# Kernel tuning notes

Hardware: AMD Instinct MI355X
Metric: run time of the kernel (lower is better)

The kernel has to match this reference:

```python
import jax, jax.numpy as jnp
import numpy as np

D = 1024
H = 8
DK = D // H
BS, NSEG, NSEN = 16, 64, 32


def _linear_params(key, d_in, d_out, scale=0.02):
    kw, kb = jax.random.split(key)
    w = jax.random.normal(kw, (d_out, d_in), dtype=jnp.float32) * scale
    b = jax.random.normal(kb, (d_out,), dtype=jnp.float32) * scale
    return w, b


def setup_inputs() -> dict:
    key = jax.random.key(0)
    ks = jax.random.split(key, 12)
    A = jax.random.normal(ks[0], (BS, NSEG, D), dtype=jnp.float32)
    V = jax.random.normal(ks[1], (BS, NSEG, D), dtype=jnp.float32)
    S = jax.random.normal(ks[2], (BS, NSEN, D), dtype=jnp.float32)
    wA, bA = _linear_params(ks[3], D, D)
    wV, bV = _linear_params(ks[4], D, D)
    wS, bS = _linear_params(ks[5], D, D)
    wq, bq = _linear_params(ks[6], D, D)
    wk, bk = _linear_params(ks[7], D, D)
    wv, bv = _linear_params(ks[8], D, D)
    w1, b1 = _linear_params(ks[9], D, D)
    w2, b2 = _linear_params(ks[10], D, D)
    return {"A": A, "V": V, "S": S,
            "wA": wA, "bA": bA, "wV": wV, "bV": bV, "wS": wS, "bS": bS,
            "wq": wq, "bq": bq, "wk": wk, "bk": bk, "wv": wv, "bv": bv,
            "w1": w1, "b1": b1, "w2": w2, "b2": b2}


def _lin(x, w, b):
    return x @ w.T + b


def reference(A, V, S, wA, bA, wV, bV, wS, bS, wq, bq, wk, bk, wv, bv, w1, b1, w2, b2):
    bs, num_seg, d_model = A.shape
    num_sen = S.shape[1]
    A = _lin(A, wA, bA)
    V = _lin(V, wV, bV)
    S = _lin(S, wS, bS)
    av = jnp.stack([A, V], axis=2)                       # (bs, num_seg, 2, d)
    q = _lin(S, wq, bq).reshape(bs, num_sen, H, DK)      # (b, s, h, dk)
    k = _lin(av, wk, bk).reshape(bs, num_seg, 2, H, DK)  # (b, g, a, h, dk)
    v = _lin(av, wv, bv).reshape(bs, num_seg, 2, H, DK)
    # attention over the size-2 A/V axis only
    attn = jnp.einsum('bshd,bgahd->bsgah', q, k) / np.sqrt(DK).astype(np.float32)
    attn = jax.nn.softmax(attn, axis=3)                  # softmax over a (A vs V)
    out = jnp.einsum('bsgah,bgahd->bsghd', attn, v)
    out = out.reshape(bs, num_sen, num_seg, d_model)
    # positionwise FF: Linear -> ReLU -> Linear (dropout p=0)
    out = _lin(jax.nn.relu(_lin(out, w1, b1)), w2, b2)
    return out
```

## Files before the change

### kernel.cpp

```cpp
#include <hip/hip_runtime.h>
#include <stdint.h>


#define D_MODEL 1024
#define N_HEAD  8
#define DK      128
#define BS      16
#define NSEG    64
#define NSEN    32

typedef __attribute__((ext_vector_type(8))) __bf16 bf16x8;
typedef __attribute__((ext_vector_type(8))) unsigned short u16x8;
typedef __attribute__((ext_vector_type(4))) float f32x4;

__device__ __forceinline__ float bf2f(unsigned short b) {
  union { unsigned int u; float f; } x; x.u = ((unsigned int)b) << 16; return x.f;
}
__device__ __forceinline__ unsigned short f2bf(float f) {
  union { float f; unsigned int u; } x; x.f = f;
  unsigned int u = x.u;
  unsigned int r = (u + 0x7fffu + ((u >> 16) & 1u)) >> 16;
  return (unsigned short)r;
}

__device__ __forceinline__ void g2l16(const void* g, void* l) {
  __builtin_amdgcn_global_load_lds(
      (const __attribute__((address_space(1))) void*)g,
      (__attribute__((address_space(3))) void*)l, 16, 0, 0);
}

struct CvtB { const float* s[11]; unsigned short* d[11]; int n4[11]; };
__global__ __launch_bounds__(256)
void cvtall_kernel(CvtB p) {
  const int z = blockIdx.y;
  const int i = blockIdx.x * 256 + threadIdx.x;
  if (i >= p.n4[z]) return;
  float4 v = reinterpret_cast<const float4*>(p.s[z])[i];
  ushort4 o;
  o.x = f2bf(v.x); o.y = f2bf(v.y); o.z = f2bf(v.z); o.w = f2bf(v.w);
  reinterpret_cast<ushort4*>(p.d[z])[i] = o;
}

struct GSeg { const unsigned short* A; const unsigned short* B;
              const float* bias; unsigned short* C; };
struct GBatch { GSeg s[3]; int end[3]; };

__global__ __launch_bounds__(256)
void gemm64_bt(GBatch gb) {
  __shared__ __align__(16) unsigned short lA[64 * 32];
  __shared__ __align__(16) unsigned short lB[128 * 32];

  const int nwg = gridDim.x;
  const int sw = (blockIdx.x & 7) * (nwg >> 3) + (blockIdx.x >> 3);
  int sgi = 0, base = 0;
  if (sw >= gb.end[0]) { sgi = 1; base = gb.end[0]; }
  if (sw >= gb.end[1]) { sgi = 2; base = gb.end[1]; }
  const GSeg sg = gb.s[sgi];
  const int st = sw - base;
  const int m0 = (st >> 3) * 64, n0 = (st & 7) * 128;

  const int t = threadIdx.x;
  const int lane = t & 63, w = t >> 6;
  const int fr = lane & 15, kg = lane >> 4;

  f32x4 acc[4][2] = {};

  const int r  = t >> 2;
  const int c8 = (t & 3) * 8;
  const unsigned short* ga  = sg.A + (size_t)(m0 + r) * 1024 + c8;
  const unsigned short* gbp = sg.B + (size_t)(n0 + r) * 1024 + c8;

  for (int k0 = 0; k0 < 1024; k0 += 32) {
    __syncthreads();
    g2l16(ga + k0,              &lA[t * 8]);
    g2l16(gbp + k0,             &lB[t * 8]);
    g2l16(gbp + k0 + 64 * 1024, &lB[2048 + t * 8]);
    __syncthreads();

    u16x8 af[4], bf[2];
#pragma unroll
    for (int mi = 0; mi < 4; ++mi)
      af[mi] = *reinterpret_cast<const u16x8*>(&lA[(mi * 16 + fr) * 32 + kg * 8]);
#pragma unroll
    for (int ni = 0; ni < 2; ++ni)
      bf[ni] = *reinterpret_cast<const u16x8*>(&lB[(w * 32 + ni * 16 + fr) * 32 + kg * 8]);
#pragma unroll
    for (int mi = 0; mi < 4; ++mi)
#pragma unroll
      for (int ni = 0; ni < 2; ++ni)
        acc[mi][ni] = __builtin_amdgcn_mfma_f32_16x16x32_bf16(
            __builtin_bit_cast(bf16x8, af[mi]), __builtin_bit_cast(bf16x8, bf[ni]),
            acc[mi][ni], 0, 0, 0);
  }

#pragma unroll
  for (int ni = 0; ni < 2; ++ni) {
    const int gn = n0 + w * 32 + ni * 16 + fr;
    const float bv = sg.bias[gn];
#pragma unroll
    for (int mi = 0; mi < 4; ++mi) {
      const int gm = m0 + mi * 16 + kg * 4;
#pragma unroll
      for (int j = 0; j < 4; ++j)
        sg.C[(size_t)(gm + j) * 1024 + gn] = f2bf(acc[mi][ni][j] + bv);
    }
  }
}

__global__ __launch_bounds__(512, 2)
void gemm8p_bt(const unsigned short* __restrict__ A, const unsigned short* __restrict__ B,
               const float* __restrict__ bias, float* __restrict__ C,
               int M, int N, int K, int nbx) {
  __shared__ __align__(16) unsigned short lds[2][2][256][64];

  const int nwg = gridDim.x;
  const int sw = (blockIdx.x & 7) * (nwg >> 3) + (blockIdx.x >> 3);
  const int m0 = (sw / nbx) * 256, n0 = (sw % nbx) * 256;

  const int T = threadIdx.x;
  const int lane = T & 63, wave = T >> 6;
  const int wr = wave >> 2, wc = wave & 3;
  const int fr = lane & 15, kg = lane >> 4;
  const int NT = K >> 6;

  const int sgs = (T & 7) ^ ((T >> 3) & 7);
  int grA[2][2], grB[2][2];
#pragma unroll
  for (int mh = 0; mh < 2; ++mh)
#pragma unroll
    for (int c = 0; c < 2; ++c) {
      int l = mh * 128 + c * 64 + (T >> 3);
      grA[mh][c] = ((l >> 6) & 1) * 128 + (l >> 7) * 64 + (l & 63);
      grB[mh][c] = ((l >> 5) & 3) * 64  + (l >> 7) * 32 + (l & 31);
    }
  const unsigned short* Abase = A + (size_t)m0 * K + sgs * 8;
  const unsigned short* Bbase = B + (size_t)n0 * K + sgs * 8;
  char* ldsc = (char*)&lds[0][0][0][0];

  auto stageA = [&](int buf, int mh, int t) {
#pragma unroll
    for (int c = 0; c < 2; ++c)
      g2l16(Abase + (size_t)grA[mh][c] * K + t * 64,
            ldsc + ((size_t)buf * 65536) + (mh * 128 + c * 64) * 128 + T * 16);
  };
  auto stageB = [&](int buf, int nh, int t) {
#pragma unroll
    for (int c = 0; c < 2; ++c)
      g2l16(Bbase + (size_t)grB[nh][c] * K + t * 64,
            ldsc + ((size_t)buf * 65536) + 32768 + (nh * 128 + c * 64) * 128 + T * 16);
  };

  int koff[2];
#pragma unroll
  for (int kk = 0; kk < 2; ++kk) koff[kk] = ((kk * 4 + kg) ^ (fr & 7)) * 16;
  int lrA[8], lrB[4];
#pragma unroll
  for (int mi = 0; mi < 8; ++mi) lrA[mi] = ((mi >> 2) * 128 + wr * 64 + (mi & 3) * 16 + fr) * 128;
#pragma unroll
  for (int ni = 0; ni < 4; ++ni) lrB[ni] = ((ni >> 1) * 128 + wc * 32 + (ni & 1) * 16 + fr) * 128;

  auto rdA = [&](int buf, int mi, int kk) -> u16x8 {
    return *reinterpret_cast<const u16x8*>(ldsc + (size_t)buf * 65536 + lrA[mi] + koff[kk]);
  };
  auto rdB = [&](int buf, int ni, int kk) -> u16x8 {
    return *reinterpret_cast<const u16x8*>(ldsc + (size_t)buf * 65536 + 32768 + lrB[ni] + koff[kk]);
  };

  f32x4 acc[8][4] = {};

  stageA(0, 0, 0); stageB(0, 0, 0); stageA(0, 1, 0); stageB(0, 1, 0);
  if (NT > 1) { stageA(1, 0, 1); stageB(1, 0, 1); stageA(1, 1, 1); }
  asm volatile("s_waitcnt vmcnt(6)" ::: "memory");
  __builtin_amdgcn_s_barrier();

  u16x8 af0[4][2], af1[4][2], bf0[2][2], bf1[2][2];

  for (int t = 0; t < NT; ++t) {
    const int buf = t & 1;
    const bool st1 = (t + 1 < NT), st2 = (t + 2 < NT);

#pragma unroll
    for (int mi = 0; mi < 4; ++mi)
#pragma unroll
      for (int kk = 0; kk < 2; ++kk) af0[mi][kk] = rdA(buf, mi, kk);
#pragma unroll
    for (int ni = 0; ni < 2; ++ni)
#pragma unroll
      for (int kk = 0; kk < 2; ++kk) bf0[ni][kk] = rdB(buf, ni, kk);
    if (st1) stageB(buf ^ 1, 1, t + 1);
    __builtin_amdgcn_s_barrier();
    asm volatile("s_waitcnt lgkmcnt(0)" ::: "memory");
    __builtin_amdgcn_sched_barrier(0);
    __builtin_amdgcn_s_setprio(1);
#pragma unroll
    for (int mi = 0; mi < 4; ++mi)
#pragma unroll
      for (int ni = 0; ni < 2; ++ni)
#pragma unroll
        for (int kk = 0; kk < 2; ++kk)
          acc[mi][ni] = __builtin_amdgcn_mfma_f32_16x16x32_bf16(
              __builtin_bit_cast(bf16x8, af0[mi][kk]), __builtin_bit_cast(bf16x8, bf0[ni][kk]),
              acc[mi][ni], 0, 0, 0);
    __builtin_amdgcn_s_setprio(0);
    __builtin_amdgcn_s_barrier();

#pragma unroll
    for (int mi = 0; mi < 4; ++mi)
#pragma unroll
      for (int kk = 0; kk < 2; ++kk) af1[mi][kk] = rdA(buf, mi + 4, kk);
#pragma unroll
    for (int ni = 0; ni < 2; ++ni)
#pragma unroll
      for (int kk = 0; kk < 2; ++kk) bf1[ni][kk] = rdB(buf, ni + 2, kk);
    if (st2) stageA(buf, 0, t + 2);
    __builtin_amdgcn_s_barrier();
    asm volatile("s_waitcnt lgkmcnt(0)" ::: "memory");
    __builtin_amdgcn_sched_barrier(0);
    __builtin_amdgcn_s_setprio(1);
#pragma unroll
    for (int mi = 0; mi < 4; ++mi)
#pragma unroll
      for (int ni = 0; ni < 2; ++ni)
#pragma unroll
        for (int kk = 0; kk < 2; ++kk)
          acc[mi][ni + 2] = __builtin_amdgcn_mfma_f32_16x16x32_bf16(
              __builtin_bit_cast(bf16x8, af0[mi][kk]), __builtin_bit_cast(bf16x8, bf1[ni][kk]),
              acc[mi][ni + 2], 0, 0, 0);
    __builtin_amdgcn_s_setprio(0);
    __builtin_amdgcn_s_barrier();

    if (st2) stageB(buf, 0, t + 2);
    __builtin_amdgcn_s_barrier();
    __builtin_amdgcn_s_setprio(1);
#pragma unroll
    for (int mi = 0; mi < 4; ++mi)
#pragma unroll
      for (int ni = 0; ni < 2; ++ni)
#pragma unroll
        for (int kk = 0; kk < 2; ++kk)
          acc[mi + 4][ni + 2] = __builtin_amdgcn_mfma_f32_16x16x32_bf16(
              __builtin_bit_cast(bf16x8, af1[mi][kk]), __builtin_bit_cast(bf16x8, bf1[ni][kk]),
              acc[mi + 4][ni + 2], 0, 0, 0);
    __builtin_amdgcn_s_setprio(0);
    __builtin_amdgcn_s_barrier();

    if (st2) stageA(buf, 1, t + 2);
    __builtin_amdgcn_s_barrier();
    __builtin_amdgcn_s_setprio(1);
#pragma unroll
    for (int mi = 0; mi < 4; ++mi)
#pragma unroll
      for (int ni = 0; ni < 2; ++ni)
#pragma unroll
        for (int kk = 0; kk < 2; ++kk)
          acc[mi + 4][ni] = __builtin_amdgcn_mfma_f32_16x16x32_bf16(
              __builtin_bit_cast(bf16x8, af1[mi][kk]), __builtin_bit_cast(bf16x8, bf0[ni][kk]),
              acc[mi + 4][ni], 0, 0, 0);
    __builtin_amdgcn_s_setprio(0);
    if (st2)       asm volatile("s_waitcnt vmcnt(6)" ::: "memory");
    else if (st1)  asm volatile("s_waitcnt vmcnt(0)" ::: "memory");
    __builtin_amdgcn_s_barrier();
  }

#pragma unroll
  for (int ni = 0; ni < 4; ++ni) {
    const int gn = n0 + wc * 64 + ni * 16 + fr;
    const float bv = bias[gn];
#pragma unroll
    for (int mi = 0; mi < 8; ++mi) {
      const int gm = m0 + wr * 128 + mi * 16 + kg * 4;
#pragma unroll
      for (int j = 0; j < 4; ++j)
        C[(size_t)(gm + j) * N + gn] = acc[mi][ni][j] + bv;
    }
  }
}

__global__ __launch_bounds__(256)
void uav_gemm(const unsigned short* __restrict__ vAV, const unsigned short* __restrict__ w1,
              unsigned short* __restrict__ UAV) {
  __shared__ __align__(16) unsigned short lA[128 * 32];
  __shared__ __align__(16) unsigned short lB[128 * 32];

  const int zb = blockIdx.z;
  const int tensor = zb >> 3, h = zb & 7;
  const unsigned short* Ab = vAV + (size_t)tensor * (1024 * 1024) + h * 128;
  const unsigned short* Bb = w1 + h * 128;
  unsigned short* Cb = UAV + (size_t)tensor * (1024 * 8192) + h * 1024;

  const int t = threadIdx.x;
  const int m0 = blockIdx.y * 128, n0 = blockIdx.x * 128;
  const int lane = t & 63, wv = t >> 6;
  const int wrow = (wv >> 1) * 64, wcol = (wv & 1) * 64;
  const int fr = lane & 15, kg = lane >> 4;

  f32x4 acc[4][4] = {};

  const int r  = t >> 2;
  const int c8 = (t & 3) * 8;
  const unsigned short* ga = Ab + (size_t)(m0 + r) * 1024 + c8;
  const unsigned short* gb = Bb + (size_t)(n0 + r) * 1024 + c8;

  for (int k0 = 0; k0 < 128; k0 += 32) {
    __syncthreads();
    g2l16(ga + k0,             &lA[t * 8]);
    g2l16(ga + k0 + 64 * 1024, &lA[2048 + t * 8]);
    g2l16(gb + k0,             &lB[t * 8]);
    g2l16(gb + k0 + 64 * 1024, &lB[2048 + t * 8]);
    __syncthreads();

    u16x8 af[4], bg_[4];
#pragma unroll
    for (int mi = 0; mi < 4; ++mi)
      af[mi] = *reinterpret_cast<const u16x8*>(&lA[(wrow + mi * 16 + fr) * 32 + kg * 8]);
#pragma unroll
    for (int ni = 0; ni < 4; ++ni)
      bg_[ni] = *reinterpret_cast<const u16x8*>(&lB[(wcol + ni * 16 + fr) * 32 + kg * 8]);
#pragma unroll
    for (int mi = 0; mi < 4; ++mi)
#pragma unroll
      for (int ni = 0; ni < 4; ++ni)
        acc[mi][ni] = __builtin_amdgcn_mfma_f32_16x16x32_bf16(
            __builtin_bit_cast(bf16x8, af[mi]), __builtin_bit_cast(bf16x8, bg_[ni]),
            acc[mi][ni], 0, 0, 0);
  }

  const int rg = kg * 4;
#pragma unroll
  for (int ni = 0; ni < 4; ++ni) {
    const int gn = n0 + wcol + ni * 16 + fr;
#pragma unroll
    for (int mi = 0; mi < 4; ++mi) {
      const int gm = m0 + wrow + mi * 16 + rg;
#pragma unroll
      for (int j = 0; j < 4; ++j)
        Cb[(size_t)(gm + j) * 8192 + gn] = f2bf(acc[mi][ni][j]);
    }
  }
}

__global__ __launch_bounds__(256)
void score_hid_kernel(const unsigned short* __restrict__ q,
                      const unsigned short* __restrict__ kAV,
                      const unsigned short* __restrict__ UAV,
                      const float* __restrict__ b1,
                      unsigned short* __restrict__ hid) {
  const int bg = blockIdx.x;
  const int b = bg >> 6, g = bg & 63;
  __shared__ float sk[2][D_MODEL];
  __shared__ float pAl[NSEN][N_HEAD];
  const size_t rowA = (size_t)bg * D_MODEL;
  const size_t rowV = rowA + (size_t)BS * NSEG * D_MODEL;
  for (int i = threadIdx.x; i < D_MODEL; i += 256) {
    sk[0][i] = bf2f(kAV[rowA + i]);
    sk[1][i] = bf2f(kAV[rowV + i]);
  }
  __syncthreads();

  const int h = threadIdx.x >> 5;
  const int l = threadIdx.x & 31;
  const float scale = 0.08838834764831845f;

  for (int s = 0; s < NSEN; ++s) {
    const unsigned short* pq = q + ((size_t)(b * NSEN + s)) * D_MODEL + h * DK;
    float la = 0.f, lv = 0.f;
#pragma unroll
    for (int e = 0; e < 4; ++e) {
      int d = l + e * 32;
      float qv = bf2f(pq[d]);
      la += qv * sk[0][h * DK + d];
      lv += qv * sk[1][h * DK + d];
    }
#pragma unroll
    for (int off = 16; off; off >>= 1) {
      la += __shfl_xor(la, off, 32);
      lv += __shfl_xor(lv, off, 32);
    }
    if (l == 0) pAl[s][h] = 1.f / (1.f + __expf((lv - la) * scale));
  }
  __syncthreads();

  const int n0 = threadIdx.x * 4;
  const unsigned short* ua = UAV + (size_t)bg * 8192 + n0;
  const unsigned short* uv = ua + (size_t)1024 * 8192;

  float dU[N_HEAD][4];
  float base[4];
#pragma unroll
  for (int j = 0; j < 4; ++j) base[j] = b1[n0 + j];
#pragma unroll
  for (int hh = 0; hh < N_HEAD; ++hh) {
    ushort4 a4 = *reinterpret_cast<const ushort4*>(ua + hh * 1024);
    ushort4 v4 = *reinterpret_cast<const ushort4*>(uv + hh * 1024);
    float va[4] = {bf2f(a4.x), bf2f(a4.y), bf2f(a4.z), bf2f(a4.w)};
    float vv[4] = {bf2f(v4.x), bf2f(v4.y), bf2f(v4.z), bf2f(v4.w)};
#pragma unroll
    for (int j = 0; j < 4; ++j) { dU[hh][j] = va[j] - vv[j]; base[j] += vv[j]; }
  }

  for (int s = 0; s < NSEN; ++s) {
    float val[4] = {base[0], base[1], base[2], base[3]};
#pragma unroll
    for (int hh = 0; hh < N_HEAD; ++hh) {
      const float p = pAl[s][hh];
#pragma unroll
      for (int j = 0; j < 4; ++j) val[j] = fmaf(p, dU[hh][j], val[j]);
    }
    ushort4 o;
    o.x = f2bf(val[0] > 0.f ? val[0] : 0.f);
    o.y = f2bf(val[1] > 0.f ? val[1] : 0.f);
    o.z = f2bf(val[2] > 0.f ? val[2] : 0.f);
    o.w = f2bf(val[3] > 0.f ? val[3] : 0.f);
    size_t orow = ((size_t)(b * NSEN + s) * NSEG + g) * D_MODEL + n0;
    *reinterpret_cast<ushort4*>(hid + orow) = o;
  }
}

extern "C" void kernel_launch(void* const* d_in, const int* in_sizes, int n_in,
                              void* d_out, int out_size, void* d_ws, size_t ws_size,
                              hipStream_t stream) {
  const float* A  = (const float*)d_in[0];
  const float* V  = (const float*)d_in[1];
  const float* S  = (const float*)d_in[2];
  const float* wA = (const float*)d_in[3];  const float* bA = (const float*)d_in[4];
  const float* wV = (const float*)d_in[5];  const float* bV = (const float*)d_in[6];
  const float* wS = (const float*)d_in[7];  const float* bS = (const float*)d_in[8];
  const float* wq = (const float*)d_in[9];  const float* bq = (const float*)d_in[10];
  const float* wk = (const float*)d_in[11]; const float* bk = (const float*)d_in[12];
  const float* wv = (const float*)d_in[13]; const float* bv = (const float*)d_in[14];
  const float* w1 = (const float*)d_in[15]; const float* b1 = (const float*)d_in[16];
  const float* w2 = (const float*)d_in[17]; const float* b2 = (const float*)d_in[18];

  const int nAV = BS * NSEG * D_MODEL;
  const int nS  = BS * NSEN * D_MODEL;
  const int nW  = D_MODEL * D_MODEL;
  const int nCT = BS * NSEN * NSEG * D_MODEL;
  const int nU  = 2 * 1024 * 8 * 1024;

  char* ws = (char*)d_ws;
  size_t off = 0;
  auto carve = [&](size_t elems) {
    unsigned short* p = (unsigned short*)(ws + off);
    off += elems * sizeof(unsigned short);
    return p;
  };
  unsigned short* bwA = carve(nW);
  unsigned short* bwV = carve(nW);
  unsigned short* bwS = carve(nW);
  unsigned short* bwq = carve(nW);
  unsigned short* bwk = carve(nW);
  unsigned short* bwv = carve(nW);
  unsigned short* bw1 = carve(nW);
  unsigned short* bw2 = carve(nW);
  unsigned short* xA  = carve(nAV);
  unsigned short* xV  = carve(nAV);
  unsigned short* xS  = carve(nS);
  unsigned short* A1V1 = carve(2 * nAV);
  unsigned short* S1  = carve(nS);
  unsigned short* qb  = carve(nS);
  unsigned short* kAV = carve(2 * nAV);
  unsigned short* vAV = carve(2 * nAV);
  unsigned short* UAV = carve(nU);
  unsigned short* hid = carve(nCT);
  (void)ws_size; (void)n_in; (void)in_sizes; (void)out_size;

  CvtB cv;
  cv.s[0] = wA; cv.d[0] = bwA; cv.n4[0] = nW / 4;
  cv.s[1] = wV; cv.d[1] = bwV; cv.n4[1] = nW / 4;
  cv.s[2] = wS; cv.d[2] = bwS; cv.n4[2] = nW / 4;
  cv.s[3] = wq; cv.d[3] = bwq; cv.n4[3] = nW / 4;
  cv.s[4] = wk; cv.d[4] = bwk; cv.n4[4] = nW / 4;
  cv.s[5] = wv; cv.d[5] = bwv; cv.n4[5] = nW / 4;
  cv.s[6] = w1; cv.d[6] = bw1; cv.n4[6] = nW / 4;
  cv.s[7] = w2; cv.d[7] = bw2; cv.n4[7] = nW / 4;
  cv.s[8] = A;  cv.d[8] = xA;  cv.n4[8] = nAV / 4;
  cv.s[9] = V;  cv.d[9] = xV;  cv.n4[9] = nAV / 4;
  cv.s[10] = S; cv.d[10] = xS; cv.n4[10] = nS / 4;
  cvtall_kernel<<<dim3(1024, 11), dim3(256), 0, stream>>>(cv);

  GBatch pj;
  pj.s[0] = {xA, bwA, bA, A1V1};        pj.end[0] = 128;
  pj.s[1] = {xV, bwV, bV, A1V1 + nAV};  pj.end[1] = 256;
  pj.s[2] = {xS, bwS, bS, S1};          pj.end[2] = 320;
  gemm64_bt<<<dim3(320), 256, 0, stream>>>(pj);

  GBatch qkv;
  qkv.s[0] = {S1,   bwq, bq, qb};   qkv.end[0] = 64;
  qkv.s[1] = {A1V1, bwk, bk, kAV};  qkv.end[1] = 320;
  qkv.s[2] = {A1V1, bwv, bv, vAV};  qkv.end[2] = 576;
  gemm64_bt<<<dim3(576), 256, 0, stream>>>(qkv);

  uav_gemm<<<dim3(8, 8, 16), dim3(256), 0, stream>>>(vAV, bw1, UAV);

  score_hid_kernel<<<dim3(BS * NSEG), dim3(256), 0, stream>>>(qb, kAV, UAV, b1, hid);

  gemm8p_bt<<<dim3(512), 512, 0, stream>>>(hid, bw2, b2, (float*)d_out,
                                           32768, 1024, 1024, 4);
}
```

Measured before the change: 198.3 us.

## Double-buffer small GEMMs and swap MFMA operands for vectorized row-contiguous stores

gemm64_bt and uav_gemm now stage the next K-slice into a second LDS buffer while computing the current one, so load latency overlaps MFMA work. All three GEMMs swap the MFMA A/B operands, which transposes the accumulator layout so each lane holds four consecutive columns. The epilogues can then use float4 bias loads and 8/16-byte vector stores instead of scalar strided stores. The large GEMM's phase order is also reshuffled so af1 is loaded later. This doubles LDS use in the small kernels, which may lower occupancy.

```diff
diff --git a/kernel.cpp b/kernel.cpp
--- a/kernel.cpp
+++ b/kernel.cpp
@@ -47,8 +47,8 @@
 
 __global__ __launch_bounds__(256)
 void gemm64_bt(GBatch gb) {
-  __shared__ __align__(16) unsigned short lA[64 * 32];
-  __shared__ __align__(16) unsigned short lB[128 * 32];
+  __shared__ __align__(16) unsigned short lA[2][64 * 32];
+  __shared__ __align__(16) unsigned short lB[2][128 * 32];
 
   const int nwg = gridDim.x;
   const int sw = (blockIdx.x & 7) * (nwg >> 3) + (blockIdx.x >> 3);
@@ -63,46 +63,59 @@
   const int lane = t & 63, w = t >> 6;
   const int fr = lane & 15, kg = lane >> 4;
 
-  f32x4 acc[4][2] = {};
+  f32x4 acc[2][4] = {};
 
   const int r  = t >> 2;
   const int c8 = (t & 3) * 8;
   const unsigned short* ga  = sg.A + (size_t)(m0 + r) * 1024 + c8;
   const unsigned short* gbp = sg.B + (size_t)(n0 + r) * 1024 + c8;
 
+  auto stage = [&](int buf, int k0) {
+    g2l16(ga + k0,              &lA[buf][t * 8]);
+    g2l16(gbp + k0,             &lB[buf][t * 8]);
+    g2l16(gbp + k0 + 64 * 1024, &lB[buf][2048 + t * 8]);
+  };
+
+  stage(0, 0);
+  asm volatile("s_waitcnt vmcnt(0)" ::: "memory");
+  __syncthreads();
+
   for (int k0 = 0; k0 < 1024; k0 += 32) {
+    const int buf = (k0 >> 5) & 1;
+    if (k0 + 32 < 1024) stage(buf ^ 1, k0 + 32);
+
+    u16x8 af[4], bf[2];
+#pragma unroll
+    for (int mi = 0; mi < 4; ++mi)
+      af[mi] = *reinterpret_cast<const u16x8*>(&lA[buf][(mi * 16 + fr) * 32 + kg * 8]);
+#pragma unroll
+    for (int ni = 0; ni < 2; ++ni)
+      bf[ni] = *reinterpret_cast<const u16x8*>(&lB[buf][(w * 32 + ni * 16 + fr) * 32 + kg * 8]);
+#pragma unroll
+    for (int ni = 0; ni < 2; ++ni)
+#pragma unroll
+      for (int mi = 0; mi < 4; ++mi)
+        acc[ni][mi] = __builtin_amdgcn_mfma_f32_16x16x32_bf16(
+            __builtin_bit_cast(bf16x8, bf[ni]), __builtin_bit_cast(bf16x8, af[mi]),
+            acc[ni][mi], 0, 0, 0);
+
+    asm volatile("s_waitcnt vmcnt(0)" ::: "memory");
     __syncthreads();
-    g2l16(ga + k0,              &lA[t * 8]);
-    g2l16(gbp + k0,             &lB[t * 8]);
-    g2l16(gbp + k0 + 64 * 1024, &lB[2048 + t * 8]);
-    __syncthreads();
-
-    u16x8 af[4], bf[2];
-#pragma unroll
-    for (int mi = 0; mi < 4; ++mi)
-      af[mi] = *reinterpret_cast<const u16x8*>(&lA[(mi * 16 + fr) * 32 + kg * 8]);
-#pragma unroll
-    for (int ni = 0; ni < 2; ++ni)
-      bf[ni] = *reinterpret_cast<const u16x8*>(&lB[(w * 32 + ni * 16 + fr) * 32 + kg * 8]);
-#pragma unroll
-    for (int mi = 0; mi < 4; ++mi)
-#pragma unroll
-      for (int ni = 0; ni < 2; ++ni)
-        acc[mi][ni] = __builtin_amdgcn_mfma_f32_16x16x32_bf16(
-            __builtin_bit_cast(bf16x8, af[mi]), __builtin_bit_cast(bf16x8, bf[ni]),
-            acc[mi][ni], 0, 0, 0);
   }
 
 #pragma unroll
   for (int ni = 0; ni < 2; ++ni) {
-    const int gn = n0 + w * 32 + ni * 16 + fr;
-    const float bv = sg.bias[gn];
+    const int gn0 = n0 + w * 32 + ni * 16 + kg * 4;
+    const float4 bv = *reinterpret_cast<const float4*>(&sg.bias[gn0]);
 #pragma unroll
     for (int mi = 0; mi < 4; ++mi) {
-      const int gm = m0 + mi * 16 + kg * 4;
-#pragma unroll
-      for (int j = 0; j < 4; ++j)
-        sg.C[(size_t)(gm + j) * 1024 + gn] = f2bf(acc[mi][ni][j] + bv);
+      const int gm = m0 + mi * 16 + fr;
+      ushort4 o;
+      o.x = f2bf(acc[ni][mi][0] + bv.x);
+      o.y = f2bf(acc[ni][mi][1] + bv.y);
+      o.z = f2bf(acc[ni][mi][2] + bv.z);
+      o.w = f2bf(acc[ni][mi][3] + bv.w);
+      *reinterpret_cast<ushort4*>(&sg.C[(size_t)gm * 1024 + gn0]) = o;
     }
   }
 }
@@ -166,7 +179,7 @@
     return *reinterpret_cast<const u16x8*>(ldsc + (size_t)buf * 65536 + 32768 + lrB[ni] + koff[kk]);
   };
 
-  f32x4 acc[8][4] = {};
+  f32x4 acc[4][8] = {};
 
   stageA(0, 0, 0); stageB(0, 0, 0); stageA(0, 1, 0); stageB(0, 1, 0);
   if (NT > 1) { stageA(1, 0, 1); stageB(1, 0, 1); stageA(1, 1, 1); }
@@ -193,21 +206,17 @@
     __builtin_amdgcn_sched_barrier(0);
     __builtin_amdgcn_s_setprio(1);
 #pragma unroll
-    for (int mi = 0; mi < 4; ++mi)
-#pragma unroll
-      for (int ni = 0; ni < 2; ++ni)
+    for (int ni = 0; ni < 2; ++ni)
+#pragma unroll
+      for (int mi = 0; mi < 4; ++mi)
 #pragma unroll
         for (int kk = 0; kk < 2; ++kk)
-          acc[mi][ni] = __builtin_amdgcn_mfma_f32_16x16x32_bf16(
-              __builtin_bit_cast(bf16x8, af0[mi][kk]), __builtin_bit_cast(bf16x8, bf0[ni][kk]),
-              acc[mi][ni], 0, 0, 0);
+          acc[ni][mi] = __builtin_amdgcn_mfma_f32_16x16x32_bf16(
+              __builtin_bit_cast(bf16x8, bf0[ni][kk]), __builtin_bit_cast(bf16x8, af0[mi][kk]),
+              acc[ni][mi], 0, 0, 0);
     __builtin_amdgcn_s_setprio(0);
     __builtin_amdgcn_s_barrier();
 
-#pragma unroll
-    for (int mi = 0; mi < 4; ++mi)
-#pragma unroll
-      for (int kk = 0; kk < 2; ++kk) af1[mi][kk] = rdA(buf, mi + 4, kk);
 #pragma unroll
     for (int ni = 0; ni < 2; ++ni)
 #pragma unroll
@@ -218,44 +227,50 @@
     __builtin_amdgcn_sched_barrier(0);
     __builtin_amdgcn_s_setprio(1);
 #pragma unroll
+    for (int ni = 0; ni < 2; ++ni)
+#pragma unroll
+      for (int mi = 0; mi < 4; ++mi)
+#pragma unroll
+        for (int kk = 0; kk < 2; ++kk)
+          acc[ni + 2][mi] = __builtin_amdgcn_mfma_f32_16x16x32_bf16(
+              __builtin_bit_cast(bf16x8, bf1[ni][kk]), __builtin_bit_cast(bf16x8, af0[mi][kk]),
+              acc[ni + 2][mi], 0, 0, 0);
+    __builtin_amdgcn_s_setprio(0);
+    __builtin_amdgcn_s_barrier();
+
+#pragma unroll
     for (int mi = 0; mi < 4; ++mi)
 #pragma unroll
-      for (int ni = 0; ni < 2; ++ni)
+      for (int kk = 0; kk < 2; ++kk) af1[mi][kk] = rdA(buf, mi + 4, kk);
+    if (st2) stageB(buf, 0, t + 2);
+    __builtin_amdgcn_s_barrier();
+    asm volatile("s_waitcnt lgkmcnt(0)" ::: "memory");
+    __builtin_amdgcn_sched_barrier(0);
+    __builtin_amdgcn_s_setprio(1);
+#pragma unroll
+    for (int ni = 0; ni < 2; ++ni)
+#pragma unroll
+      for (int mi = 0; mi < 4; ++mi)
 #pragma unroll
         for (int kk = 0; kk < 2; ++kk)
-          acc[mi][ni + 2] = __builtin_amdgcn_mfma_f32_16x16x32_bf16(
-              __builtin_bit_cast(bf16x8, af0[mi][kk]), __builtin_bit_cast(bf16x8, bf1[ni][kk]),
-              acc[mi][ni + 2], 0, 0, 0);
+          acc[ni + 2][mi + 4] = __builtin_amdgcn_mfma_f32_16x16x32_bf16(
+              __builtin_bit_cast(bf16x8, bf1[ni][kk]), __builtin_bit_cast(bf16x8, af1[mi][kk]),
+              acc[ni + 2][mi + 4], 0, 0, 0);
     __builtin_amdgcn_s_setprio(0);
     __builtin_amdgcn_s_barrier();
 
-    if (st2) stageB(buf, 0, t + 2);
+    if (st2) stageA(buf, 1, t + 2);
     __builtin_amdgcn_s_barrier();
     __builtin_amdgcn_s_setprio(1);
 #pragma unroll
-    for (int mi = 0; mi < 4; ++mi)
-#pragma unroll
-      for (int ni = 0; ni < 2; ++ni)
+    for (int ni = 0; ni < 2; ++ni)
+#pragma unroll
+      for (int mi = 0; mi < 4; ++mi)
 #pragma unroll
         for (int kk = 0; kk < 2; ++kk)
-          acc[mi + 4][ni + 2] = __builtin_amdgcn_mfma_f32_16x16x32_bf16(
-              __builtin_bit_cast(bf16x8, af1[mi][kk]), __builtin_bit_cast(bf16x8, bf1[ni][kk]),
-              acc[mi + 4][ni + 2], 0, 0, 0);
-    __builtin_amdgcn_s_setprio(0);
-    __builtin_amdgcn_s_barrier();
-
-    if (st2) stageA(buf, 1, t + 2);
-    __builtin_amdgcn_s_barrier();
-    __builtin_amdgcn_s_setprio(1);
-#pragma unroll
-    for (int mi = 0; mi < 4; ++mi)
-#pragma unroll
-      for (int ni = 0; ni < 2; ++ni)
-#pragma unroll
-        for (int kk = 0; kk < 2; ++kk)
-          acc[mi + 4][ni] = __builtin_amdgcn_mfma_f32_16x16x32_bf16(
-              __builtin_bit_cast(bf16x8, af1[mi][kk]), __builtin_bit_cast(bf16x8, bf0[ni][kk]),
-              acc[mi + 4][ni], 0, 0, 0);
+          acc[ni][mi + 4] = __builtin_amdgcn_mfma_f32_16x16x32_bf16(
+              __builtin_bit_cast(bf16x8, bf0[ni][kk]), __builtin_bit_cast(bf16x8, af1[mi][kk]),
+              acc[ni][mi + 4], 0, 0, 0);
     __builtin_amdgcn_s_setprio(0);
     if (st2)       asm volatile("s_waitcnt vmcnt(6)" ::: "memory");
     else if (st1)  asm volatile("s_waitcnt vmcnt(0)" ::: "memory");
@@ -264,14 +279,17 @@
 
 #pragma unroll
   for (int ni = 0; ni < 4; ++ni) {
-    const int gn = n0 + wc * 64 + ni * 16 + fr;
-    const float bv = bias[gn];
+    const int gn0 = n0 + wc * 64 + ni * 16 + kg * 4;
+    const float4 bv = *reinterpret_cast<const float4*>(&bias[gn0]);
 #pragma unroll
     for (int mi = 0; mi < 8; ++mi) {
-      const int gm = m0 + wr * 128 + mi * 16 + kg * 4;
-#pragma unroll
-      for (int j = 0; j < 4; ++j)
-        C[(size_t)(gm + j) * N + gn] = acc[mi][ni][j] + bv;
+      const int gm = m0 + wr * 128 + mi * 16 + fr;
+      float4 o;
+      o.x = acc[ni][mi][0] + bv.x;
+      o.y = acc[ni][mi][1] + bv.y;
+      o.z = acc[ni][mi][2] + bv.z;
+      o.w = acc[ni][mi][3] + bv.w;
+      *reinterpret_cast<float4*>(&C[(size_t)gm * N + gn0]) = o;
     }
   }
 }
@@ -279,8 +297,8 @@
 __global__ __launch_bounds__(256)
 void uav_gemm(const unsigned short* __restrict__ vAV, const unsigned short* __restrict__ w1,
               unsigned short* __restrict__ UAV) {
-  __shared__ __align__(16) unsigned short lA[128 * 32];
-  __shared__ __align__(16) unsigned short lB[128 * 32];
+  __shared__ __align__(16) unsigned short lA[2][128 * 32];
+  __shared__ __align__(16) unsigned short lB[2][128 * 32];
 
   const int zb = blockIdx.z;
   const int tensor = zb >> 3, h = zb & 7;
@@ -301,40 +319,52 @@
   const unsigned short* ga = Ab + (size_t)(m0 + r) * 1024 + c8;
   const unsigned short* gb = Bb + (size_t)(n0 + r) * 1024 + c8;
 
+  auto stage = [&](int buf, int k0) {
+    g2l16(ga + k0,             &lA[buf][t * 8]);
+    g2l16(ga + k0 + 64 * 1024, &lA[buf][2048 + t * 8]);
+    g2l16(gb + k0,             &lB[buf][t * 8]);
+    g2l16(gb + k0 + 64 * 1024, &lB[buf][2048 + t * 8]);
+  };
+
+  stage(0, 0);
+  asm volatile("s_waitcnt vmcnt(0)" ::: "memory");
+  __syncthreads();
+
   for (int k0 = 0; k0 < 128; k0 += 32) {
+    const int buf = (k0 >> 5) & 1;
+    if (k0 + 32 < 128) stage(buf ^ 1, k0 + 32);
+
+    u16x8 af[4], bg_[4];
+#pragma unroll
+    for (int mi = 0; mi < 4; ++mi)
+      af[mi] = *reinterpret_cast<const u16x8*>(&lA[buf][(wrow + mi * 16 + fr) * 32 + kg * 8]);
+#pragma unroll
+    for (int ni = 0; ni < 4; ++ni)
+      bg_[ni] = *reinterpret_cast<const u16x8*>(&lB[buf][(wcol + ni * 16 + fr) * 32 + kg * 8]);
+#pragma unroll
+    for (int ni = 0; ni < 4; ++ni)
+#pragma unroll
+      for (int mi = 0; mi < 4; ++mi)
+        acc[ni][mi] = __builtin_amdgcn_mfma_f32_16x16x32_bf16(
+            __builtin_bit_cast(bf16x8, bg_[ni]), __builtin_bit_cast(bf16x8, af[mi]),
+            acc[ni][mi], 0, 0, 0);
+
+    asm volatile("s_waitcnt vmcnt(0)" ::: "memory");
     __syncthreads();
-    g2l16(ga + k0,             &lA[t * 8]);
-    g2l16(ga + k0 + 64 * 1024, &lA[2048 + t * 8]);
-    g2l16(gb + k0,             &lB[t * 8]);
-    g2l16(gb + k0 + 64 * 1024, &lB[2048 + t * 8]);
-    __syncthreads();
-
-    u16x8 af[4], bg_[4];
-#pragma unroll
-    for (int mi = 0; mi < 4; ++mi)
-      af[mi] = *reinterpret_cast<const u16x8*>(&lA[(wrow + mi * 16 + fr) * 32 + kg * 8]);
-#pragma unroll
-    for (int ni = 0; ni < 4; ++ni)
-      bg_[ni] = *reinterpret_cast<const u16x8*>(&lB[(wcol + ni * 16 + fr) * 32 + kg * 8]);
-#pragma unroll
-    for (int mi = 0; mi < 4; ++mi)
-#pragma unroll
-      for (int ni = 0; ni < 4; ++ni)
-        acc[mi][ni] = __builtin_amdgcn_mfma_f32_16x16x32_bf16(
-            __builtin_bit_cast(bf16x8, af[mi]), __builtin_bit_cast(bf16x8, bg_[ni]),
-            acc[mi][ni], 0, 0, 0);
-  }
-
-  const int rg = kg * 4;
+  }
+
 #pragma unroll
   for (int ni = 0; ni < 4; ++ni) {
-    const int gn = n0 + wcol + ni * 16 + fr;
+    const int gn0 = n0 + wcol + ni * 16 + kg * 4;
 #pragma unroll
     for (int mi = 0; mi < 4; ++mi) {
-      const int gm = m0 + wrow + mi * 16 + rg;
-#pragma unroll
-      for (int j = 0; j < 4; ++j)
-        Cb[(size_t)(gm + j) * 8192 + gn] = f2bf(acc[mi][ni][j]);
+      const int gm = m0 + wrow + mi * 16 + fr;
+      ushort4 o;
+      o.x = f2bf(acc[ni][mi][0]);
+      o.y = f2bf(acc[ni][mi][1]);
+      o.z = f2bf(acc[ni][mi][2]);
+      o.w = f2bf(acc[ni][mi][3]);
+      *reinterpret_cast<ushort4*>(&Cb[(size_t)gm * 8192 + gn0]) = o;
     }
   }
 }
```

Result: slower. 204.5 us (+3.1%).
